# Performance work log

Measured on AMD Instinct MI355X. Metric: run time of the kernel, lower is better.

## Reference

```python
import jax, jax.numpy as jnp
import numpy as np

B, CIN, COUT, H, W = 8, 256, 256, 64, 64


def setup_inputs() -> dict:
    key = jax.random.key(0)
    k1, k2, k3 = jax.random.split(key, 3)
    x = jax.random.normal(k1, (B, CIN, H, W), dtype=jnp.float32)
    style = jax.random.normal(k2, (B, CIN), dtype=jnp.float32)
    # kaiming_normal_ (fan_in = CIN*3*3, gain = sqrt(2))
    fan_in = CIN * 9
    weight = jax.random.normal(k3, (COUT, CIN, 3, 3), dtype=jnp.float32) * np.sqrt(2.0 / fan_in)
    return {"x": x, "style": style, "weight": weight}


def reference(x, style, weight):
    b, cin, h, w = x.shape
    cout = weight.shape[0]
    # modulate: [B, Cout, Cin, 3, 3]
    mw = style[:, None, :, None, None] * weight[None]
    # demodulate
    sigma = jnp.sqrt(jnp.sum(mw * mw, axis=(2, 3, 4), keepdims=True) + 1e-8)
    dw = mw / sigma
    # per-sample conv via grouped convolution (groups = B)
    x_g = x.reshape(1, b * cin, h, w)
    w_g = dw.reshape(b * cout, cin, 3, 3)
    out = jax.lax.conv_general_dilated(
        x_g, w_g,
        window_strides=(1, 1),
        padding=((1, 1), (1, 1)),
        feature_group_count=b,
        dimension_numbers=("NCHW", "OIHW", "NCHW"),
    )
    return out.reshape(b, cout, h, w)
```

## Files before the change

kernel.cpp:

```cpp
#include <hip/hip_runtime.h>

#define B_ 8
#define CIN_ 256
#define COUT_ 256

typedef short short8_t __attribute__((ext_vector_type(8)));
typedef float float4_t __attribute__((ext_vector_type(4)));

#define DWA_SHORTS   (B_ * 9 * 32 * COUT_ * 8)
#define XPRE_SHORTS  (B_ * 8 * 66 * 66 * 32)

__device__ __forceinline__ unsigned short f2bf(float f) {
    union { float f; unsigned u; } v; v.f = f;
    unsigned u = v.u;
    unsigned r = (u + 0x7fffu + ((u >> 16) & 1u)) >> 16;
    return (unsigned short)r;
}

__device__ __forceinline__ void gload_lds16(const unsigned short* g, unsigned short* l) {
    __builtin_amdgcn_global_load_lds(
        (__attribute__((address_space(1))) void*)(g),
        (__attribute__((address_space(3))) void*)(l), 16, 0, 0);
}

__global__ __launch_bounds__(256) void k_prep(const float* __restrict__ x,
                                              const float* __restrict__ style,
                                              const float* __restrict__ weight,
                                              unsigned short* __restrict__ xpre,
                                              unsigned short* __restrict__ dwA) {
    const int blk = blockIdx.x;
    const int t = threadIdx.x;

    if (blk >= 64) {
        const int e = blk - 64;
        const int hp = e % 33;
        const int q2 = e / 33;
        const int cb = q2 & 7, b = q2 >> 3;
        const float* xslab = x + ((size_t)(b * CIN_ + cb * 32)) * 4096;
        unsigned short* dst_slab = xpre + ((size_t)(b * 8 + cb) * 66) * 2112;

#pragma unroll
        for (int rr = 0; rr < 2; ++rr) {
            const int h_out = hp * 2 + rr;
            const int h_in = h_out - 1;
            unsigned short* dst_row = dst_slab + (size_t)h_out * 2112;
#pragma unroll
            for (int pass = 0; pass < 2; ++pass) {
                int p = t + pass * 256;
                if (p >= 264) break;
                int w_out = p >> 2, g = p & 3;
                int w_in = w_out - 1;
                short8_t v = (short8_t){0, 0, 0, 0, 0, 0, 0, 0};
                if ((unsigned)h_in < 64u && (unsigned)w_in < 64u) {
                    const float* xp = xslab + ((size_t)(g * 8) * 64 + h_in) * 64 + w_in;
#pragma unroll
                    for (int j = 0; j < 8; ++j) v[j] = (short)f2bf(xp[(size_t)j * 4096]);
                }
                const int chunk = g ^ ((w_out >> 1) & 3);
                *(short8_t*)(dst_row + (size_t)w_out * 32 + chunk * 8) = v;
            }
        }
        return;
    }

    const int co_l = t >> 6;
    const int lane = t & 63;
    const int co = blk * 4 + co_l;

    float wv[4][9];
    float ss[4];
    const float* wp = weight + (size_t)co * 2304;
#pragma unroll
    for (int k = 0; k < 4; ++k) {
        float a = 0.f;
#pragma unroll
        for (int tap = 0; tap < 9; ++tap) {
            float w = wp[(lane + 64 * k) * 9 + tap];
            wv[k][tap] = w;
            a += w * w;
        }
        ss[k] = a;
    }
    float sv[8][4];
#pragma unroll
    for (int b = 0; b < 8; ++b)
#pragma unroll
        for (int k = 0; k < 4; ++k) sv[b][k] = style[b * CIN_ + lane + 64 * k];

    float inv[8];
#pragma unroll
    for (int b = 0; b < 8; ++b) {
        float part = 0.f;
#pragma unroll
        for (int k = 0; k < 4; ++k) part += sv[b][k] * sv[b][k] * ss[k];
#pragma unroll
        for (int off = 32; off > 0; off >>= 1) part += __shfl_xor(part, off, 64);
        inv[b] = 1.0f / sqrtf(part + 1e-8f);
    }

    const size_t base = (size_t)co * 8 + (lane & 7) + (size_t)(lane >> 3) * 2048;
#pragma unroll
    for (int b = 0; b < 8; ++b)
#pragma unroll
        for (int tap = 0; tap < 9; ++tap)
#pragma unroll
            for (int k = 0; k < 4; ++k) {
                size_t addr = ((size_t)(b * 9 + tap) * 32 + k * 8) * 2048 + base;
                dwA[addr] = f2bf(wv[k][tap] * sv[b][k] * inv[b]);
            }
}

__global__ __launch_bounds__(256, 2) void k_conv(const unsigned short* __restrict__ xpre,
                                                 const unsigned short* __restrict__ dwA,
                                                 float* __restrict__ out) {
    __shared__ __align__(16) unsigned short xs[2][4 * 66 * 32];

    const int b = blockIdx.x;
    const int rowgrp = blockIdx.y;
    const int co_tile = blockIdx.z;
    const int tid = threadIdx.x;
    const int lane = tid & 63, wid = tid >> 6;
    const int wave_m = wid >> 1, wave_n = wid & 1;
    const int quad = lane >> 4, l16 = lane & 15;
    const int r0 = rowgrp * 2;
    const int co_base = co_tile * 128 + wave_m * 64;

    float4_t acc[4][4];
#pragma unroll
    for (int mi = 0; mi < 4; ++mi)
#pragma unroll
        for (int ni = 0; ni < 4; ++ni) acc[mi][ni] = (float4_t){0.f, 0.f, 0.f, 0.f};

    const unsigned short* src_base = xpre + (size_t)b * 8 * 66 * 66 * 32;

    auto stage = [&](int cb, int buf) {
        const unsigned short* s = src_base + ((size_t)cb * 66 + r0) * 2112;
        unsigned short* d = xs[buf];
#pragma unroll
        for (int k = 0; k < 4; ++k)
            gload_lds16(s + (size_t)(tid + k * 256) * 8, d + (size_t)(tid + k * 256) * 8);
        if (tid < 32)
            gload_lds16(s + (size_t)(tid + 1024) * 8, d + (size_t)(tid + 1024) * 8);
    };

    short8_t abuf[3][4];
    auto loadA = [&](short8_t* dst, int acb, int atap) {
        const unsigned short* Ab = dwA + ((size_t)(b * 9 + atap) * 32 + acb * 4 + quad) * 2048
                                       + (size_t)(co_base + l16) * 8;
#pragma unroll
        for (int mi = 0; mi < 4; ++mi)
            dst[mi] = *(const short8_t*)(Ab + mi * 128);
    };

    short8_t bf[2][4];
    auto readB = [&](short8_t* dst, const unsigned short* xb, int tap) {
        const int dh = tap / 3, dwc = tap % 3;
        const unsigned short* brow = xb + (wave_n + dh) * (66 * 32);
#pragma unroll
        for (int ni = 0; ni < 4; ++ni) {
            const int col = ni * 16 + l16 + dwc;
            dst[ni] = *(const short8_t*)(brow + col * 32 + (quad ^ ((col >> 1) & 3)) * 8);
        }
    };

    stage(0, 0);
    loadA(abuf[0], 0, 0);
    loadA(abuf[1], 0, 1);

    for (int cb = 0; cb < 8; ++cb) {
        __syncthreads();
        if (cb < 7) stage(cb + 1, (cb + 1) & 1);

        const unsigned short* xb = xs[cb & 1];
        readB(bf[0], xb, 0);
#pragma unroll
        for (int tap = 0; tap < 9; ++tap) {
            const int nl = tap + 2;
            const int acb = cb + nl / 9, atap = nl % 9;
            if (acb < 8) loadA(abuf[nl % 3], acb, atap);
            if (tap < 8) readB(bf[(tap + 1) & 1], xb, tap + 1);

            const short8_t* ac = abuf[tap % 3];
            const short8_t* bc = bf[tap & 1];
            __builtin_amdgcn_s_setprio(1);
#pragma unroll
            for (int mi = 0; mi < 4; ++mi)
#pragma unroll
                for (int ni = 0; ni < 4; ++ni)
                    acc[mi][ni] = __builtin_amdgcn_mfma_f32_16x16x32_bf16(
                        ac[mi], bc[ni], acc[mi][ni], 0, 0, 0);
            __builtin_amdgcn_s_setprio(0);
        }
    }

    const int orow = r0 + wave_n;
#pragma unroll
    for (int mi = 0; mi < 4; ++mi)
#pragma unroll
        for (int ni = 0; ni < 4; ++ni)
#pragma unroll
            for (int r = 0; r < 4; ++r) {
                int co = co_base + mi * 16 + quad * 4 + r;
                int c = ni * 16 + l16;
                out[(((size_t)b * COUT_ + co) * 64 + (size_t)orow) * 64 + c] = acc[mi][ni][r];
            }
}

extern "C" void kernel_launch(void* const* d_in, const int* in_sizes, int n_in,
                              void* d_out, int out_size, void* d_ws, size_t ws_size,
                              hipStream_t stream) {
    const float* x = (const float*)d_in[0];
    const float* style = (const float*)d_in[1];
    const float* weight = (const float*)d_in[2];
    float* out = (float*)d_out;

    unsigned short* dwA = (unsigned short*)d_ws;
    unsigned short* xpre = dwA + DWA_SHORTS;

    k_prep<<<dim3(64 + B_ * 8 * 33), 256, 0, stream>>>(x, style, weight, xpre, dwA);
    k_conv<<<dim3(8, 32, 2), 256, 0, stream>>>(xpre, dwA, out);
}
```

Measured before the change: 128.6 us.

## Fuse prep and conv into one kernel with per-batch grid flag barrier

Merges the weight-demodulation/x-conversion prep kernel into the conv kernel. Each of the 64 blocks for a batch sample computes 4 output channels' demodulated weights and a share of the padded bf16 input rows, then all 64 blocks sync on a per-batch atomic counter before starting the MFMA conv. This removes one kernel launch and the gap between the two kernels, at the cost of a spin-wait barrier that relies on all 64 blocks of a batch being co-resident, plus a memset of the flags before launch.

```diff
diff --git a/kernel.cpp b/kernel.cpp
--- a/kernel.cpp
+++ b/kernel.cpp
@@ -23,103 +23,92 @@
         (__attribute__((address_space(3))) void*)(l), 16, 0, 0);
 }
 
-__global__ __launch_bounds__(256) void k_prep(const float* __restrict__ x,
-                                              const float* __restrict__ style,
-                                              const float* __restrict__ weight,
-                                              unsigned short* __restrict__ xpre,
-                                              unsigned short* __restrict__ dwA) {
-    const int blk = blockIdx.x;
-    const int t = threadIdx.x;
-
-    if (blk >= 64) {
-        const int e = blk - 64;
-        const int hp = e % 33;
-        const int q2 = e / 33;
-        const int cb = q2 & 7, b = q2 >> 3;
-        const float* xslab = x + ((size_t)(b * CIN_ + cb * 32)) * 4096;
-        unsigned short* dst_slab = xpre + ((size_t)(b * 8 + cb) * 66) * 2112;
-
-#pragma unroll
-        for (int rr = 0; rr < 2; ++rr) {
-            const int h_out = hp * 2 + rr;
-            const int h_in = h_out - 1;
-            unsigned short* dst_row = dst_slab + (size_t)h_out * 2112;
-#pragma unroll
-            for (int pass = 0; pass < 2; ++pass) {
-                int p = t + pass * 256;
-                if (p >= 264) break;
-                int w_out = p >> 2, g = p & 3;
-                int w_in = w_out - 1;
-                short8_t v = (short8_t){0, 0, 0, 0, 0, 0, 0, 0};
-                if ((unsigned)h_in < 64u && (unsigned)w_in < 64u) {
-                    const float* xp = xslab + ((size_t)(g * 8) * 64 + h_in) * 64 + w_in;
-#pragma unroll
-                    for (int j = 0; j < 8; ++j) v[j] = (short)f2bf(xp[(size_t)j * 4096]);
-                }
-                const int chunk = g ^ ((w_out >> 1) & 3);
-                *(short8_t*)(dst_row + (size_t)w_out * 32 + chunk * 8) = v;
-            }
-        }
-        return;
-    }
-
-    const int co_l = t >> 6;
-    const int lane = t & 63;
-    const int co = blk * 4 + co_l;
-
-    float wv[4][9];
-    float ss[4];
-    const float* wp = weight + (size_t)co * 2304;
-#pragma unroll
-    for (int k = 0; k < 4; ++k) {
-        float a = 0.f;
-#pragma unroll
-        for (int tap = 0; tap < 9; ++tap) {
-            float w = wp[(lane + 64 * k) * 9 + tap];
-            wv[k][tap] = w;
-            a += w * w;
-        }
-        ss[k] = a;
-    }
-    float sv[8][4];
-#pragma unroll
-    for (int b = 0; b < 8; ++b)
-#pragma unroll
-        for (int k = 0; k < 4; ++k) sv[b][k] = style[b * CIN_ + lane + 64 * k];
-
-    float inv[8];
-#pragma unroll
-    for (int b = 0; b < 8; ++b) {
-        float part = 0.f;
-#pragma unroll
-        for (int k = 0; k < 4; ++k) part += sv[b][k] * sv[b][k] * ss[k];
-#pragma unroll
-        for (int off = 32; off > 0; off >>= 1) part += __shfl_xor(part, off, 64);
-        inv[b] = 1.0f / sqrtf(part + 1e-8f);
-    }
-
-    const size_t base = (size_t)co * 8 + (lane & 7) + (size_t)(lane >> 3) * 2048;
-#pragma unroll
-    for (int b = 0; b < 8; ++b)
-#pragma unroll
-        for (int tap = 0; tap < 9; ++tap)
-#pragma unroll
-            for (int k = 0; k < 4; ++k) {
-                size_t addr = ((size_t)(b * 9 + tap) * 32 + k * 8) * 2048 + base;
-                dwA[addr] = f2bf(wv[k][tap] * sv[b][k] * inv[b]);
-            }
-}
-
-__global__ __launch_bounds__(256, 2) void k_conv(const unsigned short* __restrict__ xpre,
-                                                 const unsigned short* __restrict__ dwA,
-                                                 float* __restrict__ out) {
+__global__ __launch_bounds__(256, 2) void k_fused(const float* __restrict__ x,
+                                                  const float* __restrict__ style,
+                                                  const float* __restrict__ weight,
+                                                  unsigned short* __restrict__ xpre,
+                                                  unsigned short* __restrict__ dwA,
+                                                  float* __restrict__ out,
+                                                  int* __restrict__ flags) {
     __shared__ __align__(16) unsigned short xs[2][4 * 66 * 32];
 
     const int b = blockIdx.x;
     const int rowgrp = blockIdx.y;
     const int co_tile = blockIdx.z;
+    const int s = rowgrp * 2 + co_tile;
     const int tid = threadIdx.x;
     const int lane = tid & 63, wid = tid >> 6;
+
+    {
+        const int co = s * 4 + wid;
+        const float* wp = weight + (size_t)co * 2304;
+        float wv[4][9];
+        float ss[4];
+#pragma unroll
+        for (int k = 0; k < 4; ++k) {
+            float a = 0.f;
+#pragma unroll
+            for (int tap = 0; tap < 9; ++tap) {
+                float w = wp[(lane + 64 * k) * 9 + tap];
+                wv[k][tap] = w;
+                a += w * w;
+            }
+            ss[k] = a;
+        }
+        float sv[4];
+#pragma unroll
+        for (int k = 0; k < 4; ++k) sv[k] = style[b * CIN_ + lane + 64 * k];
+
+        float part = 0.f;
+#pragma unroll
+        for (int k = 0; k < 4; ++k) part += sv[k] * sv[k] * ss[k];
+#pragma unroll
+        for (int off = 32; off > 0; off >>= 1) part += __shfl_xor(part, off, 64);
+        const float inv = 1.0f / sqrtf(part + 1e-8f);
+
+        const size_t base = (size_t)co * 8 + (lane & 7) + (size_t)(lane >> 3) * 2048;
+#pragma unroll
+        for (int tap = 0; tap < 9; ++tap)
+#pragma unroll
+            for (int k = 0; k < 4; ++k) {
+                size_t addr = ((size_t)(b * 9 + tap) * 32 + k * 8) * 2048 + base;
+                dwA[addr] = f2bf(wv[k][tap] * sv[k] * inv);
+            }
+    }
+
+    for (int g = s; g < 528; g += 64) {
+        const int cb = g / 66, h_out = g % 66;
+        const int h_in = h_out - 1;
+        const float* xslab = x + ((size_t)(b * CIN_ + cb * 32)) * 4096;
+        unsigned short* dst_row = xpre + ((size_t)((b * 8 + cb) * 66 + h_out)) * 2112;
+#pragma unroll
+        for (int pass = 0; pass < 2; ++pass) {
+            int p = tid + pass * 256;
+            if (p >= 264) break;
+            int w_out = p >> 2, g4 = p & 3;
+            int w_in = w_out - 1;
+            short8_t v = (short8_t){0, 0, 0, 0, 0, 0, 0, 0};
+            if ((unsigned)h_in < 64u && (unsigned)w_in < 64u) {
+                const float* xp = xslab + ((size_t)(g4 * 8) * 64 + h_in) * 64 + w_in;
+#pragma unroll
+                for (int j = 0; j < 8; ++j) v[j] = (short)f2bf(xp[(size_t)j * 4096]);
+            }
+            const int chunk = g4 ^ ((w_out >> 1) & 3);
+            *(short8_t*)(dst_row + (size_t)w_out * 32 + chunk * 8) = v;
+        }
+    }
+
+    __syncthreads();
+    __threadfence();
+    if (tid == 0) {
+        __hip_atomic_fetch_add(&flags[b], 1, __ATOMIC_RELEASE, __HIP_MEMORY_SCOPE_AGENT);
+        while (__hip_atomic_load(&flags[b], __ATOMIC_ACQUIRE, __HIP_MEMORY_SCOPE_AGENT) < 64)
+            __builtin_amdgcn_s_sleep(2);
+    }
+    __syncthreads();
+    __threadfence();
+    __syncthreads();
+
     const int wave_m = wid >> 1, wave_n = wid & 1;
     const int quad = lane >> 4, l16 = lane & 15;
     const int r0 = rowgrp * 2;
@@ -134,13 +123,13 @@
     const unsigned short* src_base = xpre + (size_t)b * 8 * 66 * 66 * 32;
 
     auto stage = [&](int cb, int buf) {
-        const unsigned short* s = src_base + ((size_t)cb * 66 + r0) * 2112;
+        const unsigned short* sp = src_base + ((size_t)cb * 66 + r0) * 2112;
         unsigned short* d = xs[buf];
 #pragma unroll
         for (int k = 0; k < 4; ++k)
-            gload_lds16(s + (size_t)(tid + k * 256) * 8, d + (size_t)(tid + k * 256) * 8);
+            gload_lds16(sp + (size_t)(tid + k * 256) * 8, d + (size_t)(tid + k * 256) * 8);
         if (tid < 32)
-            gload_lds16(s + (size_t)(tid + 1024) * 8, d + (size_t)(tid + 1024) * 8);
+            gload_lds16(sp + (size_t)(tid + 1024) * 8, d + (size_t)(tid + 1024) * 8);
     };
 
     short8_t abuf[3][4];
@@ -216,7 +205,9 @@
 
     unsigned short* dwA = (unsigned short*)d_ws;
     unsigned short* xpre = dwA + DWA_SHORTS;
-
-    k_prep<<<dim3(64 + B_ * 8 * 33), 256, 0, stream>>>(x, style, weight, xpre, dwA);
-    k_conv<<<dim3(8, 32, 2), 256, 0, stream>>>(xpre, dwA, out);
-}
+    int* flags = (int*)(xpre + XPRE_SHORTS);
+
+    hipMemsetAsync(flags, 0, B_ * sizeof(int), stream);
+
+    k_fused<<<dim3(8, 32, 2), 256, 0, stream>>>(x, style, weight, xpre, dwA, out, flags);
+}
```

After: 255.5 us. 98.7% more time.
